# Kernel tuning notes

Measured on AMD Instinct MI355X. Metric: run time of the kernel, lower is better.

## Reference

```python
import jax, jax.numpy as jnp
import numpy as np

B, S, D = 4, 2048, 1024  # batch, seq_len, d_model (d_in == d_model)


def setup_inputs() -> dict:
    key = jax.random.key(0)
    ks = jax.random.split(key, 9)
    scale = 1.0 / np.sqrt(D)
    return {
        "q": jax.random.normal(ks[0], (B, S, D), jnp.float32),
        "k": jax.random.normal(ks[1], (B, S, D), jnp.float32),
        "v": jax.random.normal(ks[2], (B, S, D), jnp.float32),
        "Wq": jax.random.normal(ks[3], (D, D), jnp.float32) * scale,
        "bq": jnp.zeros((D,), jnp.float32),
        "Wk": jax.random.normal(ks[4], (D, D), jnp.float32) * scale,
        "bk": jnp.zeros((D,), jnp.float32),
        "Wv": jax.random.normal(ks[5], (D, D), jnp.float32) * scale,
        "bv": jnp.zeros((D,), jnp.float32),
    }


def reference(q, k, v, Wq, bq, Wk, bk, Wv, bv):
    query = q @ Wq + bq                      # [B, S, D]
    key_p = k @ Wk + bk                      # [B, S, D]
    value = v @ Wv + bv                      # [B, S, D]
    inv_sqrt_d = 1.0 / jnp.sqrt(jnp.asarray(D, query.dtype))
    scores = jnp.einsum('bqd,bkd->bqk', query, key_p) * inv_sqrt_d  # [B, S, S]
    w = jax.nn.softmax(scores, axis=-1)
    return jnp.einsum('bqk,bkd->bqd', w, value)  # [B, S, D]
```

## Files before the change

### kernel.cpp

```cpp
#include <hip/hip_runtime.h>
#include <math.h>


using short8  = __attribute__((ext_vector_type(8))) short;
using floatx4 = __attribute__((ext_vector_type(4))) float;

__device__ __forceinline__ unsigned short f2bf(float f) {
    union { float f; unsigned u; } x; x.f = f;
    return (unsigned short)((x.u + 0x8000u) >> 16);
}

__device__ __forceinline__ void gload_lds16(const unsigned short* g, unsigned short* l) {
    __builtin_amdgcn_global_load_lds(
        (const __attribute__((address_space(1))) unsigned int*)g,
        (__attribute__((address_space(3))) unsigned int*)l, 16, 0, 0);
}

#define SBAR   __builtin_amdgcn_s_barrier()
#define LGKM0  asm volatile("s_waitcnt lgkmcnt(0)" ::: "memory")
#define VMW(n) asm volatile("s_waitcnt vmcnt(" #n ")" ::: "memory")

__global__ __launch_bounds__(256) void prep(
    const float* __restrict__ q, const float* __restrict__ k, const float* __restrict__ v,
    const float* __restrict__ W0, const float* __restrict__ W1, const float* __restrict__ W2,
    unsigned short* __restrict__ qkvbf, unsigned short* __restrict__ Wt)
{
    __shared__ float tile[32][33];
    const int id = blockIdx.x;
    const int t  = threadIdx.x;
    if (id < 24576) {
        const int z  = id >> 13;
        const int xb = id & 8191;
        const float* x = (z == 0) ? q : (z == 1) ? k : v;
        const size_t i = ((size_t)xb * 256 + t) * 4;
        const float4 a = *(const float4*)(x + i);
        ushort4 p = { f2bf(a.x), f2bf(a.y), f2bf(a.z), f2bf(a.w) };
        *(ushort4*)(qkvbf + (size_t)z * 8192 * 1024 + i) = p;
    } else {
        const int idt = id - 24576;
        const int z  = idt >> 10;
        const int r  = idt & 1023;
        const int bx = (r & 31) * 32;
        const int by = (r >> 5) * 32;
        const float* W = (z == 0) ? W0 : (z == 1) ? W1 : W2;
        unsigned short* o = Wt + (size_t)z * 1024 * 1024;
        const int tx = t & 31;
        const int ty = (t >> 5) * 4;
        #pragma unroll
        for (int rr = 0; rr < 4; ++rr)
            tile[ty + rr][tx] = W[(size_t)(by + ty + rr) * 1024 + bx + tx];
        __syncthreads();
        #pragma unroll
        for (int rr = 0; rr < 4; ++rr)
            o[(size_t)(bx + ty + rr) * 1024 + by + tx] = f2bf(tile[tx][ty + rr]);
    }
}


#define STAGE_A(bb, kh, tt) do { \
    gload_lds16(gA + (size_t)srowA * lda + (tt) * 64 + (kh) * 32 + scol, \
                lds + (bb) * 24576 + (kh) * 4096 + t512 * 8); \
} while (0)

#define STAGE_B(bb, kh, tt) do { \
    const unsigned short* s_ = gB + (size_t)srowA * ldb + (tt) * 64 + (kh) * 32 + scol; \
    unsigned short* d_ = lds + (bb) * 24576 + 8192 + (kh) * 8192 + t512 * 8; \
    gload_lds16(s_, d_); \
    gload_lds16(s_ + (size_t)128 * ldb, d_ + 4096); \
} while (0)

#define LDSA(bb, kh, i) (*(const short8*)&lds[(bb) * 24576 + (kh) * 4096 + (arow + (i) * 16) * 32 + rslot])
#define LDSB(bb, kh, j) (*(const short8*)&lds[(bb) * 24576 + 8192 + (kh) * 8192 + (brow + (j) * 16) * 32 + rslot])

#define MFMA16 do { \
    __builtin_amdgcn_s_setprio(1); \
    _Pragma("unroll") \
    for (int i_ = 0; i_ < 4; ++i_) \
        _Pragma("unroll") \
        for (int j_ = 0; j_ < 4; ++j_) \
            acc[i_][j_] = __builtin_amdgcn_mfma_f32_16x16x32_bf16( \
                af[i_], bf[j_], acc[i_][j_], 0, 0, 0); \
    __builtin_amdgcn_s_setprio(0); \
} while (0)

__device__ __forceinline__ void gemm3buf(
    const unsigned short* __restrict__ gA, int lda,
    const unsigned short* __restrict__ gB, int ldb,
    int nt, unsigned short* lds, floatx4 (&acc)[4][4])
{
    const int t512 = threadIdx.x;
    const int lane = t512 & 63;
    const int wave = t512 >> 6;
    const int wr   = wave >> 2;
    const int wc   = wave & 3;
    const int l15  = lane & 15;
    const int quad = lane >> 4;
    const int srowA = t512 >> 2;
    const int scol  = ((t512 & 3) ^ ((t512 >> 3) & 3)) * 8;
    const int rslot = (quad ^ ((l15 >> 1) & 3)) * 8;
    const int arow  = wr * 64 + l15;
    const int brow  = wc * 64 + l15;

    short8 af[4], bf[4];

    STAGE_A(0, 0, 0); STAGE_B(0, 0, 0);
    STAGE_A(0, 1, 0); STAGE_B(0, 1, 0);
    STAGE_A(1, 0, 1); STAGE_B(1, 0, 1);
    STAGE_A(1, 1, 1); STAGE_B(1, 1, 1);
    VMW(9);
    SBAR;

    int b0 = 0, b1 = 1, b2 = 2;
    for (int t = 0; t < nt; ++t) {
        #pragma unroll
        for (int j = 0; j < 4; ++j) bf[j] = LDSB(b0, 0, j);
        #pragma unroll
        for (int i = 0; i < 4; ++i) af[i] = LDSA(b0, 0, i);
        if (t + 2 < nt) { STAGE_A(b2, 0, t + 2); STAGE_B(b2, 0, t + 2); }
        SBAR; LGKM0;
        MFMA16;
        if (t < nt - 2)       { VMW(9); }
        else if (t == nt - 2) { VMW(6); }
        else                  { VMW(0); }
        SBAR;
        #pragma unroll
        for (int j = 0; j < 4; ++j) bf[j] = LDSB(b0, 1, j);
        #pragma unroll
        for (int i = 0; i < 4; ++i) af[i] = LDSA(b0, 1, i);
        if (t + 2 < nt) { STAGE_A(b2, 1, t + 2); STAGE_B(b2, 1, t + 2); }
        SBAR; LGKM0;
        MFMA16;
        if (t < nt - 1) {
            if (t < nt - 2) { VMW(9); } else { VMW(3); }
            SBAR;
        }
        const int tmp = b0; b0 = b1; b1 = b2; b2 = tmp;
    }
}

#define EPI_IDS                                   \
    const int tt   = threadIdx.x;                 \
    const int lane = tt & 63;                     \
    const int wave = tt >> 6;                     \
    const int wr   = wave >> 2;                   \
    const int wc   = wave & 3;                    \
    const int l15  = lane & 15;                   \
    const int quad = lane >> 4;

__global__ __launch_bounds__(512) void proj8(
    const unsigned short* __restrict__ Abf,
    const unsigned short* __restrict__ Wt,
    const float* __restrict__ bq, const float* __restrict__ bk, const float* __restrict__ bv,
    unsigned short* __restrict__ Qp, unsigned short* __restrict__ Kp,
    unsigned short* __restrict__ Vpt)
{
    __shared__ __attribute__((aligned(16))) unsigned short lds[73728];
    const int id = blockIdx.x;
    const int g  = (id & 7) * 96 + (id >> 3);
    const int z  = g >> 8;
    const int r  = g & 255;
    const int m0 = (r >> 2) * 128;
    const int n0 = (r & 3) * 256;

    const unsigned short* gA = Abf + (size_t)z * 8192 * 1024 + (size_t)m0 * 1024;
    const unsigned short* gB = Wt  + (size_t)z * 1024 * 1024 + (size_t)n0 * 1024;

    floatx4 acc[4][4] = {};
    gemm3buf(gA, 1024, gB, 1024, 16, lds, acc);

    EPI_IDS
    const float* bias = (z == 0) ? bq : (z == 1) ? bk : bv;
    #pragma unroll
    for (int j = 0; j < 4; ++j) {
        const int col = n0 + wc * 64 + j * 16 + l15;
        const float bv_ = bias[col];
        #pragma unroll
        for (int i = 0; i < 4; ++i) {
            const int row = m0 + wr * 64 + i * 16 + quad * 4;
            if (z < 2) {
                unsigned short* C = (z == 0) ? Qp : Kp;
                #pragma unroll
                for (int r2 = 0; r2 < 4; ++r2)
                    C[(size_t)(row + r2) * 1024 + col] = f2bf(acc[i][j][r2] + bv_);
            } else {
                ushort4 p = { f2bf(acc[i][j][0] + bv_), f2bf(acc[i][j][1] + bv_),
                              f2bf(acc[i][j][2] + bv_), f2bf(acc[i][j][3] + bv_) };
                *(ushort4*)&Vpt[(size_t)col * 8192 + row] = p;
            }
        }
    }
}

__global__ __launch_bounds__(512) void scores8(
    const unsigned short* __restrict__ Qp,
    const unsigned short* __restrict__ Kp,
    unsigned short* __restrict__ Pexp,
    float* __restrict__ rowsum)
{
    __shared__ __attribute__((aligned(16))) unsigned short lds[73728];
    const int id = blockIdx.x;
    const int g  = (id & 7) * 64 + (id >> 3);
    const int z  = g >> 7;
    const int r  = g & 127;
    const int m0 = (r >> 3) * 128;
    const int n0 = (r & 7) * 256;

    const unsigned short* gA = Qp + (size_t)z * 2048 * 1024 + (size_t)m0 * 1024;
    const unsigned short* gB = Kp + (size_t)z * 2048 * 1024 + (size_t)n0 * 1024;

    floatx4 acc[4][4] = {};
    gemm3buf(gA, 1024, gB, 1024, 16, lds, acc);

    EPI_IDS
    unsigned short* P = Pexp + (size_t)z * 2048 * 2048;
    float* rs = rowsum + (size_t)z * 2048;
    #pragma unroll
    for (int i = 0; i < 4; ++i) {
        const int rowb = m0 + wr * 64 + i * 16 + quad * 4;
        float sm[4] = {0.f, 0.f, 0.f, 0.f};
        #pragma unroll
        for (int j = 0; j < 4; ++j) {
            const int col = n0 + wc * 64 + j * 16 + l15;
            #pragma unroll
            for (int r2 = 0; r2 < 4; ++r2) {
                const float p = __expf(acc[i][j][r2] * 0.03125f);
                sm[r2] += p;
                P[(size_t)(rowb + r2) * 2048 + col] = f2bf(p);
            }
        }
        #pragma unroll
        for (int r2 = 0; r2 < 4; ++r2) {
            float s = sm[r2];
            s += __shfl_xor(s, 1);
            s += __shfl_xor(s, 2);
            s += __shfl_xor(s, 4);
            s += __shfl_xor(s, 8);
            if (l15 == 0)
                atomicAdd(&rs[rowb + r2], s);
        }
    }
}

__global__ __launch_bounds__(512) void pv8(
    const unsigned short* __restrict__ Pexp,
    const unsigned short* __restrict__ Vpt,
    const float* __restrict__ rowsum,
    float* __restrict__ out)
{
    __shared__ __attribute__((aligned(16))) unsigned short lds[73728];
    const int id = blockIdx.x;
    const int g  = (id & 7) * 32 + (id >> 3);
    const int z  = g >> 6;
    const int r  = g & 63;
    const int m0 = (r >> 2) * 128;
    const int n0 = (r & 3) * 256;

    const unsigned short* gA = Pexp + (size_t)z * 2048 * 2048 + (size_t)m0 * 2048;
    const unsigned short* gB = Vpt  + (size_t)n0 * 8192 + (size_t)z * 2048;

    floatx4 acc[4][4] = {};
    gemm3buf(gA, 2048, gB, 8192, 32, lds, acc);

    EPI_IDS
    const float* rs = rowsum + (size_t)z * 2048;
    float* C = out + (size_t)z * 2048 * 1024;
    #pragma unroll
    for (int i = 0; i < 4; ++i) {
        const int rowb = m0 + wr * 64 + i * 16 + quad * 4;
        float inv[4];
        #pragma unroll
        for (int r2 = 0; r2 < 4; ++r2) inv[r2] = 1.0f / rs[rowb + r2];
        #pragma unroll
        for (int j = 0; j < 4; ++j) {
            const int col = n0 + wc * 64 + j * 16 + l15;
            #pragma unroll
            for (int r2 = 0; r2 < 4; ++r2)
                C[(size_t)(rowb + r2) * 1024 + col] = acc[i][j][r2] * inv[r2];
        }
    }
}

extern "C" void kernel_launch(void* const* d_in, const int* in_sizes, int n_in,
                              void* d_out, int out_size, void* d_ws, size_t ws_size,
                              hipStream_t stream)
{
    const float* q  = (const float*)d_in[0];
    const float* k  = (const float*)d_in[1];
    const float* v  = (const float*)d_in[2];
    const float* Wq = (const float*)d_in[3];
    const float* bq = (const float*)d_in[4];
    const float* Wk = (const float*)d_in[5];
    const float* bk = (const float*)d_in[6];
    const float* Wv = (const float*)d_in[7];
    const float* bv = (const float*)d_in[8];
    float* out = (float*)d_out;

    const int Bn = 4, S = 2048;

    char* w = (char*)d_ws;
    unsigned short* Wt     = (unsigned short*)(w);
    unsigned short* Qp     = (unsigned short*)(w + (6u << 20));
    unsigned short* Kp     = (unsigned short*)(w + (22u << 20));
    unsigned short* Vpt    = (unsigned short*)(w + (38u << 20));
    unsigned short* qkvbf  = (unsigned short*)(w + (54u << 20));
    unsigned short* Pexp   = (unsigned short*)(w + (54u << 20));
    float*          rowsum = (float*)(w + (86u << 20));

    hipMemsetAsync(rowsum, 0, (size_t)Bn * S * sizeof(float), stream);

    prep<<<dim3(27648), dim3(256), 0, stream>>>(q, k, v, Wq, Wk, Wv, qkvbf, Wt);

    proj8<<<dim3(768), dim3(512), 0, stream>>>(qkvbf, Wt, bq, bk, bv, Qp, Kp, Vpt);

    scores8<<<dim3(512), dim3(512), 0, stream>>>(Qp, Kp, Pexp, rowsum);

    pv8<<<dim3(256), dim3(512), 0, stream>>>(Pexp, Vpt, rowsum, out);
}
```

Baseline: 302.8 us.

## Double-buffer register fragments to overlap LDS reads with MFMA in GEMM loop

Restructures the shared GEMM main loop to hold two sets of A/B register fragments, issuing the LDS reads for the next k-half before running MFMAs on the current one. The full lgkmcnt(0) waits become partial waits (lgkmcnt(8)), and sched_barrier pins the instruction order, so LDS latency is hidden behind matrix math. Global vmcnt waits and barriers are reshuffled to match. This doubles fragment register use and makes the wait-count accounting more fragile.

After: 303.2 us. About the same (+0.1%).

```diff
diff --git a/kernel.cpp b/kernel.cpp
--- a/kernel.cpp
+++ b/kernel.cpp
@@ -16,9 +16,10 @@
         (__attribute__((address_space(3))) unsigned int*)l, 16, 0, 0);
 }
 
-#define SBAR   __builtin_amdgcn_s_barrier()
-#define LGKM0  asm volatile("s_waitcnt lgkmcnt(0)" ::: "memory")
-#define VMW(n) asm volatile("s_waitcnt vmcnt(" #n ")" ::: "memory")
+#define SBAR    __builtin_amdgcn_s_barrier()
+#define SCHEDB  __builtin_amdgcn_sched_barrier(0)
+#define LGKM(n) asm volatile("s_waitcnt lgkmcnt(" #n ")" ::: "memory")
+#define VMW(n)  asm volatile("s_waitcnt vmcnt(" #n ")" ::: "memory")
 
 __global__ __launch_bounds__(256) void prep(
     const float* __restrict__ q, const float* __restrict__ k, const float* __restrict__ v,
@@ -72,18 +73,25 @@
 #define LDSA(bb, kh, i) (*(const short8*)&lds[(bb) * 24576 + (kh) * 4096 + (arow + (i) * 16) * 32 + rslot])
 #define LDSB(bb, kh, j) (*(const short8*)&lds[(bb) * 24576 + 8192 + (kh) * 8192 + (brow + (j) * 16) * 32 + rslot])
 
-#define MFMA16 do { \
+#define READ8(dA, dB, bb, kh) do { \
+    _Pragma("unroll") \
+    for (int j_ = 0; j_ < 4; ++j_) dB[j_] = LDSB(bb, kh, j_); \
+    _Pragma("unroll") \
+    for (int i_ = 0; i_ < 4; ++i_) dA[i_] = LDSA(bb, kh, i_); \
+} while (0)
+
+#define MFMA16(Af, Bf) do { \
     __builtin_amdgcn_s_setprio(1); \
     _Pragma("unroll") \
     for (int i_ = 0; i_ < 4; ++i_) \
         _Pragma("unroll") \
         for (int j_ = 0; j_ < 4; ++j_) \
             acc[i_][j_] = __builtin_amdgcn_mfma_f32_16x16x32_bf16( \
-                af[i_], bf[j_], acc[i_][j_], 0, 0, 0); \
+                Af[i_], Bf[j_], acc[i_][j_], 0, 0, 0); \
     __builtin_amdgcn_s_setprio(0); \
 } while (0)
 
-__device__ __forceinline__ void gemm3buf(
+__device__ __forceinline__ void gemm_pipe(
     const unsigned short* __restrict__ gA, int lda,
     const unsigned short* __restrict__ gB, int ldb,
     int nt, unsigned short* lds, floatx4 (&acc)[4][4])
@@ -101,7 +109,7 @@
     const int arow  = wr * 64 + l15;
     const int brow  = wc * 64 + l15;
 
-    short8 af[4], bf[4];
+    short8 cA[4], cB[4], nA[4], nB[4];
 
     STAGE_A(0, 0, 0); STAGE_B(0, 0, 0);
     STAGE_A(0, 1, 0); STAGE_B(0, 1, 0);
@@ -109,30 +117,28 @@
     STAGE_A(1, 1, 1); STAGE_B(1, 1, 1);
     VMW(9);
     SBAR;
+    READ8(cA, cB, 0, 0);
+    VMW(6);
+    SBAR;
 
     int b0 = 0, b1 = 1, b2 = 2;
     for (int t = 0; t < nt; ++t) {
-        #pragma unroll
-        for (int j = 0; j < 4; ++j) bf[j] = LDSB(b0, 0, j);
-        #pragma unroll
-        for (int i = 0; i < 4; ++i) af[i] = LDSA(b0, 0, i);
+        READ8(nA, nB, b0, 1);
         if (t + 2 < nt) { STAGE_A(b2, 0, t + 2); STAGE_B(b2, 0, t + 2); }
-        SBAR; LGKM0;
-        MFMA16;
-        if (t < nt - 2)       { VMW(9); }
-        else if (t == nt - 2) { VMW(6); }
-        else                  { VMW(0); }
-        SBAR;
-        #pragma unroll
-        for (int j = 0; j < 4; ++j) bf[j] = LDSB(b0, 1, j);
-        #pragma unroll
-        for (int i = 0; i < 4; ++i) af[i] = LDSA(b0, 1, i);
-        if (t + 2 < nt) { STAGE_A(b2, 1, t + 2); STAGE_B(b2, 1, t + 2); }
-        SBAR; LGKM0;
-        MFMA16;
-        if (t < nt - 1) {
-            if (t < nt - 2) { VMW(9); } else { VMW(3); }
+        LGKM(8); SCHEDB;
+        MFMA16(cA, cB);
+        if (t + 1 < nt) {
+            if (t + 2 < nt) { VMW(6); } else { VMW(3); }
             SBAR;
+            READ8(cA, cB, b1, 0);
+            if (t + 2 < nt) { STAGE_A(b2, 1, t + 2); STAGE_B(b2, 1, t + 2); }
+            LGKM(8); SCHEDB;
+            MFMA16(nA, nB);
+            if (t + 2 < nt) { VMW(6); } else { VMW(0); }
+            SBAR;
+        } else {
+            LGKM(0); SCHEDB;
+            MFMA16(nA, nB);
         }
         const int tmp = b0; b0 = b1; b1 = b2; b2 = tmp;
     }
@@ -166,7 +172,7 @@
     const unsigned short* gB = Wt  + (size_t)z * 1024 * 1024 + (size_t)n0 * 1024;
 
     floatx4 acc[4][4] = {};
-    gemm3buf(gA, 1024, gB, 1024, 16, lds, acc);
+    gemm_pipe(gA, 1024, gB, 1024, 16, lds, acc);
 
     EPI_IDS
     const float* bias = (z == 0) ? bq : (z == 1) ? bk : bv;
@@ -209,7 +215,7 @@
     const unsigned short* gB = Kp + (size_t)z * 2048 * 1024 + (size_t)n0 * 1024;
 
     floatx4 acc[4][4] = {};
-    gemm3buf(gA, 1024, gB, 1024, 16, lds, acc);
+    gemm_pipe(gA, 1024, gB, 1024, 16, lds, acc);
 
     EPI_IDS
     unsigned short* P = Pexp + (size_t)z * 2048 * 2048;
@@ -259,7 +265,7 @@
     const unsigned short* gB = Vpt  + (size_t)n0 * 8192 + (size_t)z * 2048;
 
     floatx4 acc[4][4] = {};
-    gemm3buf(gA, 2048, gB, 8192, 32, lds, acc);
+    gemm_pipe(gA, 2048, gB, 8192, 32, lds, acc);
 
     EPI_IDS
     const float* rs = rowsum + (size_t)z * 2048;
```
